# Optimization experiments

Measured on AMD Instinct MI355X. Metric: run time of the kernel, lower is better.

## Reference

```python
import jax, jax.numpy as jnp
import numpy as np
import math

B, S, D, H, F = 2, 2048, 1024, 16, 4096
HD = D // H
EPS = 1e-5

def _alibi_slopes(n_heads):
    # n_heads is a power of 2 here (16): m_i = start * start**i, start = 2^(-2^(-(log2(n)-3)))
    start = 2.0 ** (-(2.0 ** (-(math.log2(n_heads) - 3))))
    return np.array([start * (start ** i) for i in range(n_heads)], dtype=np.float32)

SLOPES = jnp.asarray(_alibi_slopes(H))  # (H,)


def setup_inputs() -> dict:
    key = jax.random.key(0)
    ks = jax.random.split(key, 8)
    s = 0.02
    return {
        "x":  jax.random.normal(ks[0], (B, S, D), jnp.float32),
        "Wq": jax.random.normal(ks[1], (D, D), jnp.float32) * s,
        "Wk": jax.random.normal(ks[2], (D, D), jnp.float32) * s,
        "Wv": jax.random.normal(ks[3], (D, D), jnp.float32) * s,
        "Wo": jax.random.normal(ks[4], (D, D), jnp.float32) * s,
        "bo": jnp.zeros((D,), jnp.float32),
        "W1": jax.random.normal(ks[5], (F, D), jnp.float32) * s,
        "b1": jnp.zeros((F,), jnp.float32),
        "W2": jax.random.normal(ks[6], (D, F), jnp.float32) * s,
        "b2": jnp.zeros((D,), jnp.float32),
        "g1": jnp.ones((D,), jnp.float32),
        "be1": jnp.zeros((D,), jnp.float32),
        "g2": jnp.ones((D,), jnp.float32),
        "be2": jnp.zeros((D,), jnp.float32),
    }


def _layernorm(h, g, b):
    mu = jnp.mean(h, axis=-1, keepdims=True)
    var = jnp.mean((h - mu) ** 2, axis=-1, keepdims=True)
    return (h - mu) * jax.lax.rsqrt(var + EPS) * g + b


def reference(x, Wq, Wk, Wv, Wo, bo, W1, b1, W2, b2, g1, be1, g2, be2):
    # --- pre-norm ALiBi attention ---
    h = _layernorm(x, g1, be1)
    q = (h @ Wq.T).reshape(B, S, H, HD).transpose(0, 2, 1, 3)  # (B,H,S,HD)
    k = (h @ Wk.T).reshape(B, S, H, HD).transpose(0, 2, 1, 3)
    v = (h @ Wv.T).reshape(B, S, H, HD).transpose(0, 2, 1, 3)
    scores = jnp.einsum("bhqd,bhkd->bhqk", q, k) / math.sqrt(HD)
    pos = jnp.arange(S)
    dist = (pos[None, :] - pos[:, None]).astype(jnp.float32)      # (S,S): j - i
    bias = SLOPES[:, None, None] * dist[None, :, :]               # (H,S,S)
    attn = jax.nn.softmax(scores + bias[None], axis=-1)
    ao = jnp.einsum("bhqk,bhkd->bhqd", attn, v)
    ao = ao.transpose(0, 2, 1, 3).reshape(B, S, D) @ Wo.T + bo
    x = x + ao
    # --- pre-norm FFN ---
    h2 = _layernorm(x, g2, be2)
    ff = jax.nn.relu(h2 @ W1.T + b1) @ W2.T + b2
    return x + ff
```

## Files before the change

kernel.cpp:

```cpp
#include <hip/hip_runtime.h>
#include <hip/hip_bf16.h>
#include <stdint.h>

typedef unsigned short u16;
typedef __attribute__((ext_vector_type(8))) short short8;
typedef __attribute__((ext_vector_type(4))) float f32x4;

#define S_LEN 2048
#define D_DIM 1024
#define NHEAD 16
#define HDIM 64
#define NROWS 4096

__device__ __forceinline__ u16 f2bf(float f) {
  union { float f; uint32_t u; } c; c.f = f;
  uint32_t r = (c.u + 0x7fffu + ((c.u >> 16) & 1u)) >> 16;
  return (u16)r;
}

__device__ __forceinline__ float bf2f(u16 v) {
  union { uint32_t u; float f; } c; c.u = ((uint32_t)v) << 16;
  return c.f;
}

__device__ __forceinline__ uint32_t pack_bf2(float a, float b) {
  __hip_bfloat162 h = __float22bfloat162_rn(float2{a, b});
  union { __hip_bfloat162 h; uint32_t u; } c; c.h = h;
  return c.u;
}

__device__ __forceinline__ void gload_lds16(const void* g, void* l) {
  typedef const __attribute__((address_space(1))) unsigned int gq_t;
  typedef __attribute__((address_space(3))) unsigned int lq_t;
  __builtin_amdgcn_global_load_lds((gq_t*)(uintptr_t)g,
                                   (lq_t*)(uint32_t)(uintptr_t)l, 16, 0, 0);
}

__global__ __launch_bounds__(256) void cast_all(const float* __restrict__ Wq,
                                                const float* __restrict__ Wk,
                                                const float* __restrict__ Wv,
                                                const float* __restrict__ Wo,
                                                const float* __restrict__ W1,
                                                const float* __restrict__ W2,
                                                u16* __restrict__ wqkv,
                                                u16* __restrict__ wo,
                                                u16* __restrict__ w1,
                                                u16* __restrict__ w2) {
  int i = blockIdx.x * 256 + threadIdx.x;
  const float* src;
  u16* dst;
  int rel;
  if (i < 786432) {
    int ws = i / 262144;
    rel = i - ws * 262144;
    src = (ws == 0) ? Wq : ((ws == 1) ? Wk : Wv);
    dst = wqkv + (size_t)ws * 1048576;
  } else if (i < 1048576) {
    rel = i - 786432; src = Wo; dst = wo;
  } else if (i < 2097152) {
    rel = i - 1048576; src = W1; dst = w1;
  } else {
    rel = i - 2097152; src = W2; dst = w2;
  }
  float4 v = ((const float4*)src)[rel];
  ((ushort4*)dst)[rel] = make_ushort4(f2bf(v.x), f2bf(v.y), f2bf(v.z), f2bf(v.w));
}

__global__ __launch_bounds__(256) void ln_kernel(const float* __restrict__ x,
                                                 const float* __restrict__ g,
                                                 const float* __restrict__ be,
                                                 u16* __restrict__ out) {
  int row = blockIdx.x;
  int tid = threadIdx.x;
  const float4 v = ((const float4*)(x + (size_t)row * D_DIM))[tid];
  float s = v.x + v.y + v.z + v.w;
  float s2 = v.x * v.x + v.y * v.y + v.z * v.z + v.w * v.w;
#pragma unroll
  for (int off = 1; off < 64; off <<= 1) {
    s += __shfl_xor(s, off);
    s2 += __shfl_xor(s2, off);
  }
  __shared__ float ss[4], ss2[4];
  if ((tid & 63) == 0) { ss[tid >> 6] = s; ss2[tid >> 6] = s2; }
  __syncthreads();
  s = ss[0] + ss[1] + ss[2] + ss[3];
  s2 = ss2[0] + ss2[1] + ss2[2] + ss2[3];
  float mu = s * (1.0f / D_DIM);
  float var = s2 * (1.0f / D_DIM) - mu * mu;
  float rs = rsqrtf(var + 1e-5f);
  float4 gv = ((const float4*)g)[tid];
  float4 bv = ((const float4*)be)[tid];
  ushort4 o = make_ushort4(f2bf((v.x - mu) * rs * gv.x + bv.x),
                           f2bf((v.y - mu) * rs * gv.y + bv.y),
                           f2bf((v.z - mu) * rs * gv.z + bv.z),
                           f2bf((v.w - mu) * rs * gv.w + bv.w));
  ((ushort4*)(out + (size_t)row * D_DIM))[tid] = o;
}

template <int EPI>
__global__ __launch_bounds__(512, 2) void gemm_bt2(const u16* __restrict__ A,
                                                   const u16* __restrict__ Bw,
                                                   void* __restrict__ Cout,
                                                   const float* __restrict__ bias,
                                                   int M, int N, int K, int ksl) {
  __shared__ u16 lsA[3][256 * 32];
  __shared__ u16 lsB[3][256 * 32];
  const int tid = threadIdx.x;
  const int wid = tid >> 6, lane = tid & 63;
  const int l4 = lane & 15, lh = lane >> 4;
  const int wr = wid >> 2, wc = wid & 3;
  const int nbn = N >> 8;
  const int nwg = (M >> 8) * nbn;
  const int slice = blockIdx.x / nwg;
  const int id0 = blockIdx.x % nwg;
  const int t0 = (id0 & 7) * (nwg >> 3) + (id0 >> 3);
  const int bm = t0 / nbn, bn = t0 % nbn;
  const int Ks = K / ksl;

  f32x4 acc[8][4];
#pragma unroll
  for (int i = 0; i < 8; ++i)
#pragma unroll
    for (int j = 0; j < 4; ++j) acc[i][j] = (f32x4){0.f, 0.f, 0.f, 0.f};

  const int srow = lane >> 2;
  const int sblk = (lane & 3) ^ ((lane >> 3) & 3);
  const u16* Abase = A + ((size_t)bm * 256 + wid * 32 + srow) * K + (size_t)slice * Ks + sblk * 8;
  const u16* Bbase = Bw + ((size_t)bn * 256 + wid * 32 + srow) * K + (size_t)slice * Ks + sblk * 8;
  const size_t r16 = (size_t)16 * K;
#define STAGE(BUF, KT)                                              \
  {                                                                 \
    int ko = (KT) * 32;                                             \
    gload_lds16(Abase + ko, (char*)lsA[BUF] + wid * 2048);          \
    gload_lds16(Abase + r16 + ko, (char*)lsA[BUF] + wid * 2048 + 1024); \
    gload_lds16(Bbase + ko, (char*)lsB[BUF] + wid * 2048);          \
    gload_lds16(Bbase + r16 + ko, (char*)lsB[BUF] + wid * 2048 + 1024); \
  }

  const int swz = (lh ^ ((l4 >> 1) & 3)) << 4;
  int aoff[8], boff[4];
#pragma unroll
  for (int m = 0; m < 8; ++m) aoff[m] = (wr * 128 + m * 16 + l4) * 64 + swz;
#pragma unroll
  for (int n = 0; n < 4; ++n) boff[n] = (wc * 64 + n * 16 + l4) * 64 + swz;

  const int NT = Ks >> 5;
  STAGE(0, 0);
  STAGE(1, 1);
  asm volatile("s_waitcnt vmcnt(4)" ::: "memory");
  __builtin_amdgcn_s_barrier();
  int cb = 0, sb = 2;

  for (int t = 0; t < NT; ++t) {
    if (t + 2 < NT) STAGE(sb, t + 2);
    const char* La = (const char*)lsA[cb];
    const char* Lb = (const char*)lsB[cb];
    short8 aF[4], bF[4], aG[4];
#pragma unroll
    for (int m = 0; m < 4; ++m) aF[m] = *(const short8*)(La + aoff[m]);
#pragma unroll
    for (int n = 0; n < 4; ++n) bF[n] = *(const short8*)(Lb + boff[n]);
    __builtin_amdgcn_s_setprio(1);
#pragma unroll
    for (int m = 0; m < 4; ++m)
#pragma unroll
      for (int n = 0; n < 4; ++n)
        acc[m][n] = __builtin_amdgcn_mfma_f32_16x16x32_bf16(aF[m], bF[n], acc[m][n], 0, 0, 0);
    __builtin_amdgcn_s_setprio(0);
#pragma unroll
    for (int m = 0; m < 4; ++m) aG[m] = *(const short8*)(La + aoff[m + 4]);
    __builtin_amdgcn_s_setprio(1);
#pragma unroll
    for (int m = 0; m < 4; ++m)
#pragma unroll
      for (int n = 0; n < 4; ++n)
        acc[m + 4][n] = __builtin_amdgcn_mfma_f32_16x16x32_bf16(aG[m], bF[n], acc[m + 4][n], 0, 0, 0);
    __builtin_amdgcn_s_setprio(0);
    if (t + 1 < NT) {
      if (t + 2 < NT) {
        asm volatile("s_waitcnt vmcnt(4)" ::: "memory");
      } else {
        asm volatile("s_waitcnt vmcnt(0)" ::: "memory");
      }
      __builtin_amdgcn_s_barrier();
    }
    cb = (cb == 2) ? 0 : cb + 1;
    sb = (sb == 2) ? 0 : sb + 1;
  }

  const int row0 = bm * 256 + wr * 128 + lh * 4;
  const int col0 = bn * 256 + wc * 64 + l4;
  u16* Cp = (u16*)Cout + (size_t)slice * M * N;
#pragma unroll
  for (int m = 0; m < 8; ++m) {
#pragma unroll
    for (int n = 0; n < 4; ++n) {
      int col = col0 + n * 16;
#pragma unroll
      for (int r = 0; r < 4; ++r) {
        size_t idx = (size_t)(row0 + m * 16 + r) * N + col;
        float v = acc[m][n][r];
        if (EPI == 0) {
          ((u16*)Cout)[idx] = f2bf(v);
        } else if (EPI == 2) {
          v += bias[col];
          ((u16*)Cout)[idx] = f2bf(v > 0.f ? v : 0.f);
        } else {
          Cp[idx] = f2bf(v);
        }
      }
    }
  }
#undef STAGE
}

template <int EPI>
__global__ __launch_bounds__(256) void gemm_bt(const u16* __restrict__ A,
                                               const u16* __restrict__ Bw,
                                               void* __restrict__ Cout,
                                               const float* __restrict__ bias,
                                               const float* __restrict__ resid,
                                               int M, int N, int K, int ksl) {
  __shared__ u16 lsA[128 * 64];
  __shared__ u16 lsB[128 * 64];
  const int tid = threadIdx.x;
  const int wid = tid >> 6, lane = tid & 63;
  const int l4 = lane & 15, lh = lane >> 4;
  const int nbn = N >> 7;
  const int nwgs = (M >> 7) * nbn;
  const int slice = blockIdx.x / nwgs;
  const int id0 = blockIdx.x % nwgs;
  const int t = (id0 & 7) * (nwgs >> 3) + (id0 >> 3);
  const int bm = t / nbn, bn = t % nbn;
  const int wr = wid >> 1, wc = wid & 1;
  const int Ks = K / ksl;

  f32x4 acc[4][4];
#pragma unroll
  for (int i = 0; i < 4; ++i)
#pragma unroll
    for (int j = 0; j < 4; ++j) acc[i][j] = (f32x4){0.f, 0.f, 0.f, 0.f};

  const u16* Ab = A + (size_t)bm * 128 * K + (size_t)slice * Ks;
  const u16* Bb = Bw + (size_t)bn * 128 * K + (size_t)slice * Ks;
  const int srow = (lane >> 3);
  const int scol = (lane & 7) * 8;

  for (int k0 = 0; k0 < Ks; k0 += 64) {
#pragma unroll
    for (int c = 0; c < 4; ++c) {
      int ch = wid * 4 + c;
      int row = ch * 8 + srow;
      gload_lds16(Ab + (size_t)row * K + k0 + scol, &lsA[ch * 512]);
      gload_lds16(Bb + (size_t)row * K + k0 + scol, &lsB[ch * 512]);
    }
    __syncthreads();
#pragma unroll
    for (int ks = 0; ks < 2; ++ks) {
      short8 af[4], bf[4];
#pragma unroll
      for (int i = 0; i < 4; ++i) {
        af[i] = *(const short8*)&lsA[(wr * 64 + i * 16 + l4) * 64 + ks * 32 + lh * 8];
        bf[i] = *(const short8*)&lsB[(wc * 64 + i * 16 + l4) * 64 + ks * 32 + lh * 8];
      }
#pragma unroll
      for (int i = 0; i < 4; ++i)
#pragma unroll
        for (int j = 0; j < 4; ++j)
          acc[i][j] = __builtin_amdgcn_mfma_f32_16x16x32_bf16(af[i], bf[j], acc[i][j], 0, 0, 0);
    }
    __syncthreads();
  }

  const int row0 = bm * 128 + wr * 64;
  const int col0 = bn * 128 + wc * 64;
  float* Cp = (float*)Cout + (size_t)slice * M * N;
#pragma unroll
  for (int i = 0; i < 4; ++i) {
#pragma unroll
    for (int j = 0; j < 4; ++j) {
      int col = col0 + j * 16 + l4;
#pragma unroll
      for (int r = 0; r < 4; ++r) {
        int row = row0 + i * 16 + lh * 4 + r;
        size_t idx = (size_t)row * N + col;
        float v = acc[i][j][r];
        if (EPI == 1) {
          ((float*)Cout)[idx] = v + bias[col] + resid[idx];
        } else {
          Cp[idx] = v;
        }
      }
    }
  }
}

__global__ __launch_bounds__(256) void reduce4_kernel(const u16* __restrict__ pk,
                                                      const float* __restrict__ resid,
                                                      const float* __restrict__ bias,
                                                      float* __restrict__ out) {
  const size_t SL = (size_t)NROWS * D_DIM;
  int i = blockIdx.x * 256 + threadIdx.x;
  short8 p0 = *(const short8*)(pk + (size_t)i * 8);
  short8 p1 = *(const short8*)(pk + SL + (size_t)i * 8);
  short8 p2 = *(const short8*)(pk + 2 * SL + (size_t)i * 8);
  short8 p3 = *(const short8*)(pk + 3 * SL + (size_t)i * 8);
  int col = (i * 8) & (D_DIM - 1);
  float4 b0 = *(const float4*)(bias + col);
  float4 b1 = *(const float4*)(bias + col + 4);
  float4 r0 = ((const float4*)resid)[i * 2];
  float4 r1 = ((const float4*)resid)[i * 2 + 1];
  float o[8];
#pragma unroll
  for (int j = 0; j < 8; ++j)
    o[j] = bf2f((u16)p0[j]) + bf2f((u16)p1[j]) + bf2f((u16)p2[j]) + bf2f((u16)p3[j]);
  float4 w0 = {o[0] + b0.x + r0.x, o[1] + b0.y + r0.y, o[2] + b0.z + r0.z, o[3] + b0.w + r0.w};
  float4 w1 = {o[4] + b1.x + r1.x, o[5] + b1.y + r1.y, o[6] + b1.z + r1.z, o[7] + b1.w + r1.w};
  ((float4*)out)[i * 2] = w0;
  ((float4*)out)[i * 2 + 1] = w1;
}

__global__ __launch_bounds__(256) void transpose_v(const u16* __restrict__ qkv,
                                                   u16* __restrict__ vt) {
  const int gw = blockIdx.x * 4 + (threadIdx.x >> 6);
  const int lane = threadIdx.x & 63;
  const int bh = gw >> 5;
  const int st = gw & 31;
  const int b = bh >> 4, h = bh & 15;
  const u16* src = qkv + (size_t)(b * S_LEN + st * 64) * 3072 + 2048 + h * 64 + lane;
  short8 acc8[8];
#pragma unroll
  for (int o = 0; o < 8; ++o)
#pragma unroll
    for (int i = 0; i < 8; ++i)
      acc8[o][i] = (short)src[(size_t)(o * 8 + i) * 3072];
  u16* dst = vt + ((size_t)bh * 64 + lane) * S_LEN + st * 64;
#pragma unroll
  for (int o = 0; o < 8; ++o) *(short8*)(dst + o * 8) = acc8[o];
}

__global__ __launch_bounds__(256, 4) void attn_kernel(const u16* __restrict__ qkv,
                                                      const u16* __restrict__ vt,
                                                      u16* __restrict__ ao,
                                                      float* __restrict__ pO,
                                                      float* __restrict__ pML) {
  const int id = blockIdx.x;
  const int sub = id & 63;
  const int ugrp = id >> 6;
  int h, j;
  if (ugrp < 15) { h = 15 - ugrp / 3; j = ugrp % 3; }
  else if (ugrp < 19) { h = 10 - ((ugrp - 15) >> 1); j = (ugrp - 15) & 1; }
  else { h = 27 - ugrp; j = 0; }
  const int b = sub >> 5, qt = sub & 31;
  const int bh = b * 16 + h;
  const int tid = threadIdx.x;
  const int wid = tid >> 6, lane = tid & 63;
  const int l4 = lane & 15, lh = lane >> 4;

  __shared__ u16 Kt[2][64 * 64];
  __shared__ u16 Vt[2][64 * 64];
  __shared__ u16 Pt[4][16 * 64];

  const size_t RS = 3 * D_DIM;
  const u16* base = qkv + (size_t)b * S_LEN * RS + h * HDIM;
  const u16* kbase = base + D_DIM;
  const u16* vtb = vt + (size_t)bh * HDIM * S_LEN;
  char* PtW = (char*)Pt[wid];

  short8 qf[2];
  {
    const u16* qp = base + (size_t)(qt * 64 + wid * 16 + l4) * RS + lh * 8;
    qf[0] = *(const short8*)qp;
    qf[1] = *(const short8*)(qp + 32);
  }

  int koff[4][2];
#pragma unroll
  for (int nb = 0; nb < 4; ++nb)
#pragma unroll
    for (int ks = 0; ks < 2; ++ks) {
      int row = nb * 16 + l4;
      koff[nb][ks] = row * 128 + (((ks * 32 + lh * 8) * 2) ^ ((row & 7) << 4));
    }
  int poff[2];
#pragma unroll
  for (int ks = 0; ks < 2; ++ks)
    poff[ks] = l4 * 128 + (((ks * 64 + lh * 16)) ^ ((l4 & 7) << 4));
  int pwoff[4];
#pragma unroll
  for (int nb = 0; nb < 4; ++nb)
    pwoff[nb] = l4 * 128 + (((lh * 8 + nb * 32)) ^ ((l4 & 7) << 4));

  const float slope2 = exp2f(-0.5f * (float)(h + 1)) * 1.44269504088896f;
  const float scale2 = 0.125f * 1.44269504088896f;
  const int ibase = lh * 4 - (qt * 64 + wid * 16 + l4);
  float bc[4][4];
#pragma unroll
  for (int nb = 0; nb < 4; ++nb)
#pragma unroll
    for (int r = 0; r < 4; ++r)
      bc[nb][r] = slope2 * (float)(ibase + 16 * nb + r);

  int nt = (int)ceilf(40.0f / (64.0f * slope2)) + 1;
  if (nt > 32) nt = 32;
  const int nsp = (nt + 11) / 12;
  const int ktmin = 32 - nt;
  const int hi = 31 - j * 12;
  int lo = hi - 11;
  if (lo < ktmin) lo = ktmin;

  float m = -1e30f;
  f32x4 lacc = (f32x4){0.f, 0.f, 0.f, 0.f};
  f32x4 accO[4];
#pragma unroll
  for (int nd = 0; nd < 4; ++nd) accO[nd] = (f32x4){0.f, 0.f, 0.f, 0.f};
  const short8 vones = {(short)0x3F80, (short)0x3F80, (short)0x3F80, (short)0x3F80,
                        (short)0x3F80, (short)0x3F80, (short)0x3F80, (short)0x3F80};

  const int srow = tid >> 3;
  const int sc8 = (tid & 7) * 8;
  const int swo = srow * 128 + ((sc8 * 2) ^ ((srow & 7) << 4));
  short8 kreg[2], vreg[2];
#define STAGE_LOAD(KT)                                                              \
  {                                                                                 \
    kreg[0] = *(const short8*)(kbase + (size_t)((KT)*64 + srow) * RS + sc8);        \
    kreg[1] = *(const short8*)(kbase + (size_t)((KT)*64 + srow + 32) * RS + sc8);   \
    vreg[0] = *(const short8*)(vtb + (size_t)srow * S_LEN + (KT)*64 + sc8);         \
    vreg[1] = *(const short8*)(vtb + (size_t)(srow + 32) * S_LEN + (KT)*64 + sc8);  \
  }
#define STAGE_WRITE(B)                                   \
  {                                                      \
    *(short8*)((char*)Kt[B] + swo) = kreg[0];            \
    *(short8*)((char*)Kt[B] + swo + 4096) = kreg[1];     \
    *(short8*)((char*)Vt[B] + swo) = vreg[0];            \
    *(short8*)((char*)Vt[B] + swo + 4096) = vreg[1];     \
  }

  STAGE_LOAD(hi);
  STAGE_WRITE(0);
  __syncthreads();
  int cur = 0;
  float ktoff = slope2 * 64.0f * (float)hi;
  const float dko = slope2 * 64.0f;

  for (int kt = hi; kt >= lo; --kt) {
    if (kt > lo) STAGE_LOAD(kt - 1);
    const char* Kc = (const char*)Kt[cur];
    const char* Vc = (const char*)Vt[cur];

    f32x4 sacc[4];
#pragma unroll
    for (int nb = 0; nb < 4; ++nb) sacc[nb] = (f32x4){0.f, 0.f, 0.f, 0.f};
    __builtin_amdgcn_s_setprio(1);
#pragma unroll
    for (int ks = 0; ks < 2; ++ks)
#pragma unroll
      for (int nb = 0; nb < 4; ++nb) {
        short8 kf = *(const short8*)(Kc + koff[nb][ks]);
        sacc[nb] = __builtin_amdgcn_mfma_f32_16x16x32_bf16(kf, qf[ks], sacc[nb], 0, 0, 0);
      }
    __builtin_amdgcn_s_setprio(0);

    float p[4][4];
#pragma unroll
    for (int nb = 0; nb < 4; ++nb)
#pragma unroll
      for (int r = 0; r < 4; ++r)
        p[nb][r] = fmaf(sacc[nb][r], scale2, bc[nb][r]);

    float mx0 = fmaxf(fmaxf(p[0][0], p[0][1]), fmaxf(p[0][2], p[0][3]));
    float mx1 = fmaxf(fmaxf(p[1][0], p[1][1]), fmaxf(p[1][2], p[1][3]));
    float mx2 = fmaxf(fmaxf(p[2][0], p[2][1]), fmaxf(p[2][2], p[2][3]));
    float mx3 = fmaxf(fmaxf(p[3][0], p[3][1]), fmaxf(p[3][2], p[3][3]));
    float tm = fmaxf(fmaxf(mx0, mx1), fmaxf(mx2, mx3));
    tm = fmaxf(tm, __shfl_xor(tm, 16));
    tm = fmaxf(tm, __shfl_xor(tm, 32));

    float mm = m - ktoff;
    if (__any(tm > mm)) {
      float mn = fmaxf(mm, tm);
      float corr = exp2f(mm - mn);
      m = mn + ktoff;
      mm = mn;
      float cb[4];
#pragma unroll
      for (int r = 0; r < 4; ++r)
        cb[r] = __shfl(corr, (lane & 48) | (lh * 4 + r));
#pragma unroll
      for (int nd = 0; nd < 4; ++nd)
#pragma unroll
        for (int r = 0; r < 4; ++r) accO[nd][r] *= cb[r];
#pragma unroll
      for (int r = 0; r < 4; ++r) lacc[r] *= cb[r];
    }

#pragma unroll
    for (int nb = 0; nb < 4; ++nb)
#pragma unroll
      for (int r = 0; r < 4; ++r) p[nb][r] = exp2f(p[nb][r] - mm);

#pragma unroll
    for (int nb = 0; nb < 4; ++nb) {
      uint32_t w0 = pack_bf2(p[nb][0], p[nb][1]);
      uint32_t w1 = pack_bf2(p[nb][2], p[nb][3]);
      *(uint2*)(PtW + pwoff[nb]) = make_uint2(w0, w1);
    }
    asm volatile("s_waitcnt lgkmcnt(0)" ::: "memory");

    __builtin_amdgcn_s_setprio(1);
#pragma unroll
    for (int ks = 0; ks < 2; ++ks) {
      short8 pf = *(const short8*)(PtW + poff[ks]);
      lacc = __builtin_amdgcn_mfma_f32_16x16x32_bf16(pf, vones, lacc, 0, 0, 0);
#pragma unroll
      for (int nd = 0; nd < 4; ++nd) {
        short8 vf = *(const short8*)(Vc + koff[nd][ks]);
        accO[nd] = __builtin_amdgcn_mfma_f32_16x16x32_bf16(pf, vf, accO[nd], 0, 0, 0);
      }
    }
    __builtin_amdgcn_s_setprio(0);

    if (kt > lo) STAGE_WRITE(cur ^ 1);
    __syncthreads();
    cur ^= 1;
    ktoff -= dko;
  }

  if (nsp == 1) {
    float ib[4];
#pragma unroll
    for (int r = 0; r < 4; ++r) ib[r] = 1.0f / lacc[r];
    u16* aop = ao + ((size_t)(b * S_LEN + qt * 64 + wid * 16 + lh * 4)) * D_DIM + h * HDIM;
#pragma unroll
    for (int nd = 0; nd < 4; ++nd)
#pragma unroll
      for (int r = 0; r < 4; ++r)
        aop[(size_t)r * D_DIM + nd * 16 + l4] = f2bf(accO[nd][r] * ib[r]);
  } else {
    const int sbase = (h <= 10) ? (h - 9) * 2 : 4 + (h - 11) * 3;
    const int pidx = sub * 19 + sbase + j;
    float* Op = pO + (size_t)pidx * 4096;
#pragma unroll
    for (int nd = 0; nd < 4; ++nd)
#pragma unroll
      for (int r = 0; r < 4; ++r)
        Op[(wid * 16 + lh * 4 + r) * 64 + nd * 16 + l4] = accO[nd][r];
    float mq[4];
#pragma unroll
    for (int r = 0; r < 4; ++r)
      mq[r] = __shfl(m, (lane & 48) | (lh * 4 + r));
    if (l4 == 0) {
      float* mlp = pML + (size_t)pidx * 128 + (wid * 16 + lh * 4) * 2;
#pragma unroll
      for (int r = 0; r < 4; ++r) {
        mlp[r * 2] = mq[r];
        mlp[r * 2 + 1] = lacc[r];
      }
    }
  }
#undef STAGE_LOAD
#undef STAGE_WRITE
}

__global__ __launch_bounds__(256) void attn_combine(const float* __restrict__ pO,
                                                    const float* __restrict__ pML,
                                                    u16* __restrict__ ao) {
  const int g = blockIdx.x;
  const int sub = g & 63;
  const int h = 9 + (g >> 6);
  const int b = sub >> 5, qt = sub & 31;
  const int nsp = (h <= 10) ? 2 : 3;
  const int sbase = (h <= 10) ? (h - 9) * 2 : 4 + (h - 11) * 3;
  const int pidx0 = sub * 19 + sbase;
  const int tid = threadIdx.x;
  const int row = tid >> 2;
  const int d0 = (tid & 3) * 16;

  float mj[3], lj[3];
#pragma unroll
  for (int k = 0; k < 3; ++k) { mj[k] = -1e30f; lj[k] = 0.f; }
  for (int k = 0; k < nsp; ++k) {
    mj[k] = pML[(size_t)(pidx0 + k) * 128 + row * 2];
    lj[k] = pML[(size_t)(pidx0 + k) * 128 + row * 2 + 1];
  }
  float ms = fmaxf(mj[0], fmaxf(mj[1], mj[2]));
  float w[3];
  float lsum = 0.f;
#pragma unroll
  for (int k = 0; k < 3; ++k) {
    w[k] = exp2f(mj[k] - ms);
    lsum += w[k] * lj[k];
  }
  float inv = 1.0f / lsum;

  u16* aop = ao + ((size_t)(b * S_LEN + qt * 64 + row)) * D_DIM + h * HDIM + d0;
#pragma unroll
  for (int c = 0; c < 4; ++c) {
    float4 o = {0.f, 0.f, 0.f, 0.f};
    for (int k = 0; k < nsp; ++k) {
      const float4 v = *(const float4*)(pO + (size_t)(pidx0 + k) * 4096 + row * 64 + d0 + c * 4);
      o.x += w[k] * v.x; o.y += w[k] * v.y; o.z += w[k] * v.z; o.w += w[k] * v.w;
    }
    ushort4 u4 = make_ushort4(f2bf(o.x * inv), f2bf(o.y * inv), f2bf(o.z * inv), f2bf(o.w * inv));
    *(ushort4*)(aop + c * 4) = u4;
  }
}

extern "C" void kernel_launch(void* const* d_in, const int* in_sizes, int n_in,
                              void* d_out, int out_size, void* d_ws, size_t ws_size,
                              hipStream_t stream) {
  const float* x   = (const float*)d_in[0];
  const float* Wq  = (const float*)d_in[1];
  const float* Wk  = (const float*)d_in[2];
  const float* Wv  = (const float*)d_in[3];
  const float* Wo  = (const float*)d_in[4];
  const float* bo  = (const float*)d_in[5];
  const float* W1  = (const float*)d_in[6];
  const float* b1  = (const float*)d_in[7];
  const float* W2  = (const float*)d_in[8];
  const float* b2  = (const float*)d_in[9];
  const float* g1  = (const float*)d_in[10];
  const float* be1 = (const float*)d_in[11];
  const float* g2  = (const float*)d_in[12];
  const float* be2 = (const float*)d_in[13];

  char* p = (char*)d_ws;
  u16* wqkv = (u16*)p; p += (size_t)3072 * 1024 * 2;
  u16* wo   = (u16*)p; p += (size_t)1024 * 1024 * 2;
  u16* w1   = (u16*)p; p += (size_t)4096 * 1024 * 2;
  u16* w2   = (u16*)p; p += (size_t)4096 * 1024 * 2;
  u16* hb   = (u16*)p; p += (size_t)4096 * 1024 * 2;
  u16* qkvb = (u16*)p; p += (size_t)4096 * 3072 * 2;
  u16* aob  = (u16*)p; p += (size_t)4096 * 1024 * 2;
  float* x1 = (float*)p; p += (size_t)4096 * 1024 * 4;
  u16* h2b  = (u16*)p; p += (size_t)4096 * 1024 * 2;
  u16* ff1  = (u16*)p; p += (size_t)4096 * 4096 * 2;
  u16* vt   = ff1;
  float* pO = (float*)(ff1 + (size_t)4 * 1024 * 1024);
  float* pML = pO + (size_t)1216 * 4096;
  u16* pk = hb;

  cast_all<<<12288, 256, 0, stream>>>(Wq, Wk, Wv, Wo, W1, W2, wqkv, wo, w1, w2);

  ln_kernel<<<4096, 256, 0, stream>>>(x, g1, be1, hb);
  gemm_bt2<0><<<16 * 12, 512, 0, stream>>>(hb, wqkv, qkvb, nullptr, 4096, 3072, 1024, 1);
  transpose_v<<<256, 256, 0, stream>>>(qkvb, vt);
  attn_kernel<<<1792, 256, 0, stream>>>(qkvb, vt, aob, pO, pML);
  attn_combine<<<448, 256, 0, stream>>>(pO, pML, aob);
  gemm_bt<1><<<32 * 8, 256, 0, stream>>>(aob, wo, x1, bo, x, 4096, 1024, 1024, 1);
  ln_kernel<<<4096, 256, 0, stream>>>(x1, g2, be2, h2b);
  gemm_bt2<2><<<16 * 16, 512, 0, stream>>>(h2b, w1, ff1, b1, 4096, 4096, 1024, 1);
  gemm_bt2<3><<<4 * 64, 512, 0, stream>>>(ff1, w2, pk, nullptr, 4096, 1024, 4096, 4);
  reduce4_kernel<<<2048, 256, 0, stream>>>(pk, x1, b2, (float*)d_out);
}
```

Before: 224.2 us.

## Restructure 256x256 GEMM into K=64 double-buffered ping-pong with interleaved partial loads

Replaces the triple-buffered K=32 GEMM with a 128KB double-buffered K=64 scheme. Each iteration is split into four MFMA quadrants, and the next tile's A halves and the B halves two tiles ahead are loaded between them, separated by barriers and sched_barrier. The aim is to overlap global-to-LDS traffic with MFMA work at finer grain and to cut per-K-step loop and barrier overhead. In exchange it adds more barriers per iteration and uses the full LDS, which may limit occupancy to one block per CU despite the launch bound of two.

```diff
diff --git a/kernel.cpp b/kernel.cpp
--- a/kernel.cpp
+++ b/kernel.cpp
@@ -98,13 +98,12 @@
 }
 
 template <int EPI>
-__global__ __launch_bounds__(512, 2) void gemm_bt2(const u16* __restrict__ A,
-                                                   const u16* __restrict__ Bw,
-                                                   void* __restrict__ Cout,
-                                                   const float* __restrict__ bias,
-                                                   int M, int N, int K, int ksl) {
-  __shared__ u16 lsA[3][256 * 32];
-  __shared__ u16 lsB[3][256 * 32];
+__global__ __launch_bounds__(512, 2) void gemm8p(const u16* __restrict__ A,
+                                                 const u16* __restrict__ Bw,
+                                                 void* __restrict__ Cout,
+                                                 const float* __restrict__ bias,
+                                                 int M, int N, int K, int ksl) {
+  __shared__ char L0[131072];
   const int tid = threadIdx.x;
   const int wid = tid >> 6, lane = tid & 63;
   const int l4 = lane & 15, lh = lane >> 4;
@@ -116,6 +115,7 @@
   const int t0 = (id0 & 7) * (nwg >> 3) + (id0 >> 3);
   const int bm = t0 / nbn, bn = t0 % nbn;
   const int Ks = K / ksl;
+  const int NG = Ks >> 6;
 
   f32x4 acc[8][4];
 #pragma unroll
@@ -123,69 +123,107 @@
 #pragma unroll
     for (int j = 0; j < 4; ++j) acc[i][j] = (f32x4){0.f, 0.f, 0.f, 0.f};
 
-  const int srow = lane >> 2;
+  const int srow4 = lane >> 2;
   const int sblk = (lane & 3) ^ ((lane >> 3) & 3);
-  const u16* Abase = A + ((size_t)bm * 256 + wid * 32 + srow) * K + (size_t)slice * Ks + sblk * 8;
-  const u16* Bbase = Bw + ((size_t)bn * 256 + wid * 32 + srow) * K + (size_t)slice * Ks + sblk * 8;
-  const size_t r16 = (size_t)16 * K;
-#define STAGE(BUF, KT)                                              \
-  {                                                                 \
-    int ko = (KT) * 32;                                             \
-    gload_lds16(Abase + ko, (char*)lsA[BUF] + wid * 2048);          \
-    gload_lds16(Abase + r16 + ko, (char*)lsA[BUF] + wid * 2048 + 1024); \
-    gload_lds16(Bbase + ko, (char*)lsB[BUF] + wid * 2048);          \
-    gload_lds16(Bbase + r16 + ko, (char*)lsB[BUF] + wid * 2048 + 1024); \
+  const u16* Asrc = A + ((size_t)(bm * 256 + wid * 16 + srow4)) * K + (size_t)slice * Ks + sblk * 8;
+  const u16* Bsrc = Bw + ((size_t)(bn * 256 + wid * 16 + srow4)) * K + (size_t)slice * Ks + sblk * 8;
+  const size_t hstr = (size_t)128 * K;
+#define STG(MAT, SRC, H, KT, TB)                                             \
+  {                                                                          \
+    const u16* s_ = (SRC) + (size_t)(H) * hstr + (KT) * 64;                  \
+    char* d_ = L0 + (TB) * 65536 + (MAT) * 32768 + ((H) * 128 + wid * 16) * 64; \
+    gload_lds16(s_, d_);                                                     \
+    gload_lds16(s_ + 32, d_ + 16384);                                        \
   }
 
   const int swz = (lh ^ ((l4 >> 1) & 3)) << 4;
-  int aoff[8], boff[4];
-#pragma unroll
-  for (int m = 0; m < 8; ++m) aoff[m] = (wr * 128 + m * 16 + l4) * 64 + swz;
-#pragma unroll
-  for (int n = 0; n < 4; ++n) boff[n] = (wc * 64 + n * 16 + l4) * 64 + swz;
-
-  const int NT = Ks >> 5;
-  STAGE(0, 0);
-  STAGE(1, 1);
+  const int aB = (wr * 128 + l4) * 64 + swz;
+  const int bB = 32768 + (wc * 64 + l4) * 64 + swz;
+#define RDA(LC, M_, KS) (*(const short8*)((LC) + (KS)*16384 + (M_)*1024 + aB))
+#define RDB(LC, N_, KS) (*(const short8*)((LC) + (KS)*16384 + (N_)*1024 + bB))
+
+  STG(0, Asrc, 0, 0, 0); STG(0, Asrc, 1, 0, 0);
+  STG(1, Bsrc, 0, 0, 0); STG(1, Bsrc, 1, 0, 0);
+  STG(1, Bsrc, 0, 1, 1); STG(1, Bsrc, 1, 1, 1);
   asm volatile("s_waitcnt vmcnt(4)" ::: "memory");
   __builtin_amdgcn_s_barrier();
-  int cb = 0, sb = 2;
-
-  for (int t = 0; t < NT; ++t) {
-    if (t + 2 < NT) STAGE(sb, t + 2);
-    const char* La = (const char*)lsA[cb];
-    const char* Lb = (const char*)lsB[cb];
-    short8 aF[4], bF[4], aG[4];
-#pragma unroll
-    for (int m = 0; m < 4; ++m) aF[m] = *(const short8*)(La + aoff[m]);
-#pragma unroll
-    for (int n = 0; n < 4; ++n) bF[n] = *(const short8*)(Lb + boff[n]);
+
+  for (int g = 0; g < NG; ++g) {
+    const char* Lc = L0 + (g & 1) * 65536;
+    const int tbo = (g + 1) & 1;
+    short8 aF[4][2], aG[4][2], bF[2][2], bG[2][2];
+
+#pragma unroll
+    for (int m = 0; m < 4; ++m) { aF[m][0] = RDA(Lc, m, 0); aF[m][1] = RDA(Lc, m, 1); }
+#pragma unroll
+    for (int n = 0; n < 2; ++n) { bF[n][0] = RDB(Lc, n, 0); bF[n][1] = RDB(Lc, n, 1); }
+    if (g + 1 < NG) STG(0, Asrc, 0, g + 1, tbo);
+    __builtin_amdgcn_s_barrier();
+    asm volatile("s_waitcnt lgkmcnt(0)" ::: "memory");
+    __builtin_amdgcn_sched_barrier(0);
     __builtin_amdgcn_s_setprio(1);
 #pragma unroll
     for (int m = 0; m < 4; ++m)
 #pragma unroll
-      for (int n = 0; n < 4; ++n)
-        acc[m][n] = __builtin_amdgcn_mfma_f32_16x16x32_bf16(aF[m], bF[n], acc[m][n], 0, 0, 0);
+      for (int n = 0; n < 2; ++n) {
+        acc[m][n] = __builtin_amdgcn_mfma_f32_16x16x32_bf16(aF[m][0], bF[n][0], acc[m][n], 0, 0, 0);
+        acc[m][n] = __builtin_amdgcn_mfma_f32_16x16x32_bf16(aF[m][1], bF[n][1], acc[m][n], 0, 0, 0);
+      }
     __builtin_amdgcn_s_setprio(0);
-#pragma unroll
-    for (int m = 0; m < 4; ++m) aG[m] = *(const short8*)(La + aoff[m + 4]);
+    __builtin_amdgcn_s_barrier();
+
+#pragma unroll
+    for (int n = 0; n < 2; ++n) { bG[n][0] = RDB(Lc, n + 2, 0); bG[n][1] = RDB(Lc, n + 2, 1); }
+    if (g + 1 < NG) STG(0, Asrc, 1, g + 1, tbo);
+    __builtin_amdgcn_s_barrier();
+    asm volatile("s_waitcnt lgkmcnt(0)" ::: "memory");
+    __builtin_amdgcn_sched_barrier(0);
     __builtin_amdgcn_s_setprio(1);
 #pragma unroll
     for (int m = 0; m < 4; ++m)
 #pragma unroll
-      for (int n = 0; n < 4; ++n)
-        acc[m + 4][n] = __builtin_amdgcn_mfma_f32_16x16x32_bf16(aG[m], bF[n], acc[m + 4][n], 0, 0, 0);
+      for (int n = 0; n < 2; ++n) {
+        acc[m][n + 2] = __builtin_amdgcn_mfma_f32_16x16x32_bf16(aF[m][0], bG[n][0], acc[m][n + 2], 0, 0, 0);
+        acc[m][n + 2] = __builtin_amdgcn_mfma_f32_16x16x32_bf16(aF[m][1], bG[n][1], acc[m][n + 2], 0, 0, 0);
+      }
     __builtin_amdgcn_s_setprio(0);
-    if (t + 1 < NT) {
-      if (t + 2 < NT) {
+    __builtin_amdgcn_s_barrier();
+
+#pragma unroll
+    for (int m = 0; m < 4; ++m) { aG[m][0] = RDA(Lc, m + 4, 0); aG[m][1] = RDA(Lc, m + 4, 1); }
+    if (g + 2 < NG) STG(1, Bsrc, 0, g + 2, (g & 1));
+    __builtin_amdgcn_s_barrier();
+    asm volatile("s_waitcnt lgkmcnt(0)" ::: "memory");
+    __builtin_amdgcn_sched_barrier(0);
+    __builtin_amdgcn_s_setprio(1);
+#pragma unroll
+    for (int m = 0; m < 4; ++m)
+#pragma unroll
+      for (int n = 0; n < 2; ++n) {
+        acc[m + 4][n] = __builtin_amdgcn_mfma_f32_16x16x32_bf16(aG[m][0], bF[n][0], acc[m + 4][n], 0, 0, 0);
+        acc[m + 4][n] = __builtin_amdgcn_mfma_f32_16x16x32_bf16(aG[m][1], bF[n][1], acc[m + 4][n], 0, 0, 0);
+      }
+    __builtin_amdgcn_s_setprio(0);
+    __builtin_amdgcn_s_barrier();
+
+    if (g + 2 < NG) STG(1, Bsrc, 1, g + 2, (g & 1));
+    __builtin_amdgcn_s_setprio(1);
+#pragma unroll
+    for (int m = 0; m < 4; ++m)
+#pragma unroll
+      for (int n = 0; n < 2; ++n) {
+        acc[m + 4][n + 2] = __builtin_amdgcn_mfma_f32_16x16x32_bf16(aG[m][0], bG[n][0], acc[m + 4][n + 2], 0, 0, 0);
+        acc[m + 4][n + 2] = __builtin_amdgcn_mfma_f32_16x16x32_bf16(aG[m][1], bG[n][1], acc[m + 4][n + 2], 0, 0, 0);
+      }
+    __builtin_amdgcn_s_setprio(0);
+    if (g + 1 < NG) {
+      if (g + 2 < NG) {
         asm volatile("s_waitcnt vmcnt(4)" ::: "memory");
       } else {
         asm volatile("s_waitcnt vmcnt(0)" ::: "memory");
       }
       __builtin_amdgcn_s_barrier();
     }
-    cb = (cb == 2) ? 0 : cb + 1;
-    sb = (sb == 2) ? 0 : sb + 1;
   }
 
   const int row0 = bm * 256 + wr * 128 + lh * 4;
@@ -211,7 +249,9 @@
       }
     }
   }
-#undef STAGE
+#undef STG
+#undef RDA
+#undef RDB
 }
 
 template <int EPI>
@@ -643,13 +683,13 @@
   cast_all<<<12288, 256, 0, stream>>>(Wq, Wk, Wv, Wo, W1, W2, wqkv, wo, w1, w2);
 
   ln_kernel<<<4096, 256, 0, stream>>>(x, g1, be1, hb);
-  gemm_bt2<0><<<16 * 12, 512, 0, stream>>>(hb, wqkv, qkvb, nullptr, 4096, 3072, 1024, 1);
+  gemm8p<0><<<16 * 12, 512, 0, stream>>>(hb, wqkv, qkvb, nullptr, 4096, 3072, 1024, 1);
   transpose_v<<<256, 256, 0, stream>>>(qkvb, vt);
   attn_kernel<<<1792, 256, 0, stream>>>(qkvb, vt, aob, pO, pML);
   attn_combine<<<448, 256, 0, stream>>>(pO, pML, aob);
   gemm_bt<1><<<32 * 8, 256, 0, stream>>>(aob, wo, x1, bo, x, 4096, 1024, 1024, 1);
   ln_kernel<<<4096, 256, 0, stream>>>(x1, g2, be2, h2b);
-  gemm_bt2<2><<<16 * 16, 512, 0, stream>>>(h2b, w1, ff1, b1, 4096, 4096, 1024, 1);
-  gemm_bt2<3><<<4 * 64, 512, 0, stream>>>(ff1, w2, pk, nullptr, 4096, 1024, 4096, 4);
+  gemm8p<2><<<16 * 16, 512, 0, stream>>>(h2b, w1, ff1, b1, 4096, 4096, 1024, 1);
+  gemm8p<3><<<4 * 64, 512, 0, stream>>>(ff1, w2, pk, nullptr, 4096, 1024, 4096, 4);
   reduce4_kernel<<<2048, 256, 0, stream>>>(pk, x1, b2, (float*)d_out);
 }
```

Measured after the change: 223.8 us. Within noise of the previous version (-0.2%).
